# Kernel optimization log

Hardware: AMD Instinct MI355X
Metric: run time of the kernel (lower is better)

The kernel has to match this reference:

```python
import jax, jax.numpy as jnp
import numpy as np

N_NODES = 50000
N_EDGES = 800000
HID = 256
EDGE_DIM = 3


def setup_inputs() -> dict:
    key = jax.random.key(0)
    ks = jax.random.split(key, 10)
    h = jax.random.normal(ks[0], (N_NODES, HID), dtype=jnp.float32)
    edge_index = jax.random.randint(ks[1], (2, N_EDGES), 0, N_NODES, dtype=jnp.int64)
    edge_attr = jax.random.normal(ks[2], (N_EDGES, EDGE_DIM), dtype=jnp.float32)
    # edge_mlp: Linear(3, hid//2) -> SiLU -> Linear(hid//2, 1)
    half = HID // 2
    W1 = jax.random.normal(ks[3], (EDGE_DIM, half), dtype=jnp.float32) / np.sqrt(EDGE_DIM)
    b1 = jnp.zeros((half,), dtype=jnp.float32)
    W2 = jax.random.normal(ks[4], (half, 1), dtype=jnp.float32) / np.sqrt(half)
    b2 = jnp.zeros((1,), dtype=jnp.float32)
    # GCNConv lin (bias=False inside lin; separate additive bias)
    Wc = jax.random.normal(ks[5], (HID, HID), dtype=jnp.float32) / np.sqrt(HID)
    bc = jnp.zeros((HID,), dtype=jnp.float32)
    return {"h": h, "edge_index": edge_index, "edge_attr": edge_attr,
            "W1": W1, "b1": b1, "W2": W2, "b2": b2, "Wc": Wc, "bc": bc}


def reference(h, edge_index, edge_attr, W1, b1, W2, b2, Wc, bc):
    N = h.shape[0]
    # per-edge scalar weight in (0,1): sigmoid(MLP(edge_attr))
    t = jax.nn.silu(edge_attr @ W1 + b1)
    w = jax.nn.sigmoid((t @ W2 + b2)[:, 0])  # [E]

    # add self loops with weight 1.0
    loop = jnp.arange(N, dtype=edge_index.dtype)
    row = jnp.concatenate([edge_index[0], loop])  # sources
    col = jnp.concatenate([edge_index[1], loop])  # targets
    ew = jnp.concatenate([w, jnp.ones((N,), dtype=w.dtype)])

    # symmetric normalization (PyG gcn_norm, flow source_to_target)
    deg = jax.ops.segment_sum(ew, col, num_segments=N)
    dinv = jnp.where(deg > 0, jax.lax.rsqrt(deg), 0.0)
    norm = dinv[row] * ew * dinv[col]  # [E+N]

    # linear transform then gather-scale-scatter aggregation
    x = h @ Wc  # [N, HID]
    msg = x[row] * norm[:, None]  # [E+N, HID]
    out = jax.ops.segment_sum(msg, col, num_segments=N) + bc
    return out
```

## Files before the change

kernel.cpp:

```cpp
#include <hip/hip_runtime.h>

#define NN 50000
#define NE 800000
#define HID 256
#define HALF 128
#define NBLK ((NN + 255) / 256)
#define MT ((NN + 63) / 64)

typedef __attribute__((ext_vector_type(8))) short short8;
typedef __attribute__((ext_vector_type(4))) float floatx4;

__device__ inline unsigned short f2b(float f) {
    unsigned int u = __float_as_uint(f);
    unsigned int r = (u + 0x7FFFu + ((u >> 16) & 1u)) >> 16;
    return (unsigned short)r;
}
__device__ inline float b2f(unsigned int u) {
    return __uint_as_float(u << 16);
}

__global__ __launch_bounds__(256) void k_init(unsigned long long* __restrict__ degq) {
    int n = blockIdx.x * 256 + threadIdx.x;
    if (n < NN) degq[n] = 0ull;
}

__global__ __launch_bounds__(256) void k_convW(const float* __restrict__ Wc,
                                               unsigned short* __restrict__ Wt) {
    int t = blockIdx.x * 256 + threadIdx.x;
    int n = t >> 8, k = t & 255;
    Wt[n * 256 + k] = f2b(Wc[k * 256 + n]);
}

__global__ __launch_bounds__(256) void k_edge_mlp(
    const float* __restrict__ ea, const int* __restrict__ eidx,
    const float* __restrict__ W1, const float* __restrict__ b1,
    const float* __restrict__ W2, const float* __restrict__ b2,
    float* __restrict__ w, unsigned long long* __restrict__ degq) {
    __shared__ float4 wp[HALF];
    __shared__ float w2s[HALF];
    int tid = threadIdx.x;
    if (tid < HALF) {
        wp[tid] = make_float4(W1[tid], W1[HALF + tid], W1[2 * HALF + tid], b1[tid]);
        w2s[tid] = W2[tid];
    }
    __syncthreads();
    int e = blockIdx.x * 256 + tid;
    if (e >= NE) return;
    float a0 = ea[3 * e], a1 = ea[3 * e + 1], a2 = ea[3 * e + 2];
    float acc = b2[0];
#pragma unroll 4
    for (int j = 0; j < HALF; ++j) {
        float4 wv = wp[j];
        float t = fmaf(a0, wv.x, fmaf(a1, wv.y, fmaf(a2, wv.z, wv.w)));
        float s = t * __builtin_amdgcn_rcpf(1.0f + __expf(-t));
        acc = fmaf(s, w2s[j], acc);
    }
    float wv = __builtin_amdgcn_rcpf(1.0f + __expf(-acc));
    w[e] = wv;
    int col = eidx[NE + e];
    unsigned long long q = (1ull << 48) |
        (unsigned long long)__float2uint_rn(wv * 16777216.0f);
    atomicAdd(&degq[col], q);
}

__global__ __launch_bounds__(256) void k_scan_blk(
    const unsigned long long* __restrict__ degq, float* __restrict__ dinv,
    int* __restrict__ off, int* __restrict__ bsum) {
    __shared__ int smem[256];
    int tid = threadIdx.x;
    int idx = blockIdx.x * 256 + tid;
    int v = 0;
    if (idx < NN) {
        unsigned long long q = degq[idx];
        v = (int)(q >> 48);
        float d = fmaf((float)(q & 0xFFFFFFFFFFFFull), 5.9604644775390625e-8f, 1.0f);
        dinv[idx] = rsqrtf(d);
    }
    smem[tid] = v;
    __syncthreads();
#pragma unroll
    for (int s = 1; s < 256; s <<= 1) {
        int t = (tid >= s) ? smem[tid - s] : 0;
        __syncthreads();
        smem[tid] += t;
        __syncthreads();
    }
    if (idx < NN) off[idx] = smem[tid] - v;
    if (tid == 255) bsum[blockIdx.x] = smem[255];
}

__global__ __launch_bounds__(256) void k_scan_top(const int* __restrict__ bsum,
                                                  int* __restrict__ bpre,
                                                  int* __restrict__ off) {
    __shared__ int smem[256];
    int tid = threadIdx.x;
    int v = (tid < NBLK) ? bsum[tid] : 0;
    smem[tid] = v;
    __syncthreads();
#pragma unroll
    for (int s = 1; s < 256; s <<= 1) {
        int t = (tid >= s) ? smem[tid - s] : 0;
        __syncthreads();
        smem[tid] += t;
        __syncthreads();
    }
    if (tid < NBLK) bpre[tid] = smem[tid] - v;
    if (tid == 255) off[NN] = smem[255];
}

__global__ __launch_bounds__(256) void k_scan_add(const int* __restrict__ bpre,
                                                  int* __restrict__ off,
                                                  int* __restrict__ cursor) {
    int idx = blockIdx.x * 256 + threadIdx.x;
    if (idx < NN) {
        int o = off[idx] + bpre[blockIdx.x];
        off[idx] = o;
        cursor[idx] = o;
    }
}

__global__ __launch_bounds__(256) void k_fill(
    const int* __restrict__ eidx, const float* __restrict__ w,
    const float* __restrict__ dinv, int* __restrict__ cursor,
    unsigned int* __restrict__ epk) {
    int e = blockIdx.x * 256 + threadIdx.x;
    if (e >= NE) return;
    int row = eidx[e];
    int col = eidx[NE + e];
    int p = atomicAdd(&cursor[col], 1);
    float nm = dinv[row] * w[e] * dinv[col];
    epk[p] = (unsigned)row | ((unsigned)f2b(nm) << 16);
}

__global__ __launch_bounds__(256) void k_gemm_mfma(
    const float* __restrict__ A, const unsigned short* __restrict__ Wt,
    unsigned short* __restrict__ xh) {
    __shared__ __align__(16) unsigned short As[64][40];
    int tid = threadIdx.x;
    int wave = tid >> 6, lane = tid & 63;
    int mbase = blockIdx.x * 64;
    int nbase = wave * 64;
    int lrow = lane & 15;
    int lg = lane >> 4;
    floatx4 acc[4][4];
#pragma unroll
    for (int t = 0; t < 4; ++t)
#pragma unroll
        for (int u = 0; u < 4; ++u)
            acc[t][u] = (floatx4){0.f, 0.f, 0.f, 0.f};

    int srow = tid >> 2;
    int skg = tid & 3;
    int arow = mbase + srow;
    if (arow >= NN) arow = NN - 1;

    for (int k0 = 0; k0 < 256; k0 += 32) {
        float4 f0 = *(const float4*)&A[arow * 256 + k0 + skg * 8];
        float4 f1 = *(const float4*)&A[arow * 256 + k0 + skg * 8 + 4];
        __syncthreads();
        uint4 pk;
        pk.x = (unsigned)f2b(f0.x) | ((unsigned)f2b(f0.y) << 16);
        pk.y = (unsigned)f2b(f0.z) | ((unsigned)f2b(f0.w) << 16);
        pk.z = (unsigned)f2b(f1.x) | ((unsigned)f2b(f1.y) << 16);
        pk.w = (unsigned)f2b(f1.z) | ((unsigned)f2b(f1.w) << 16);
        *(uint4*)&As[srow][skg * 8] = pk;
        __syncthreads();

        short8 af[4], bf[4];
#pragma unroll
        for (int t = 0; t < 4; ++t)
            af[t] = *(const short8*)&As[t * 16 + lrow][lg * 8];
#pragma unroll
        for (int u = 0; u < 4; ++u)
            bf[u] = *(const short8*)&Wt[(nbase + u * 16 + lrow) * 256 + k0 + lg * 8];
#pragma unroll
        for (int t = 0; t < 4; ++t)
#pragma unroll
            for (int u = 0; u < 4; ++u)
                acc[t][u] = __builtin_amdgcn_mfma_f32_16x16x32_bf16(
                    af[t], bf[u], acc[t][u], 0, 0, 0);
    }
#pragma unroll
    for (int t = 0; t < 4; ++t) {
        int rowb = mbase + t * 16 + lg * 4;
#pragma unroll
        for (int r = 0; r < 4; ++r) {
            int row = rowb + r;
            if (row < NN) {
#pragma unroll
                for (int u = 0; u < 4; ++u)
                    xh[row * 256 + nbase + u * 16 + lrow] = f2b(acc[t][u][r]);
            }
        }
    }
}

__global__ __launch_bounds__(256) void k_aggregate(
    const unsigned short* __restrict__ xh, const int* __restrict__ off,
    const unsigned int* __restrict__ epk, const float* __restrict__ dinv,
    const float* __restrict__ bc, float* __restrict__ out) {
    int n = blockIdx.x * 4 + (threadIdx.x >> 6);
    int lane = threadIdx.x & 63;
    if (n >= NN) return;
    int c4 = lane * 4;
    float di = dinv[n];
    float s = di * di;
    ushort4 xv = *(const ushort4*)&xh[n * 256 + c4];
    float4 bv = *(const float4*)&bc[c4];
    float ax = fmaf(b2f(xv.x), s, bv.x);
    float ay = fmaf(b2f(xv.y), s, bv.y);
    float az = fmaf(b2f(xv.z), s, bv.z);
    float aw = fmaf(b2f(xv.w), s, bv.w);
    int jb = off[n], je = off[n + 1];
    int j = jb;
    for (; j + 4 <= je; j += 4) {
        unsigned p0 = epk[j], p1 = epk[j + 1], p2 = epk[j + 2], p3 = epk[j + 3];
        ushort4 v0 = *(const ushort4*)&xh[(p0 & 0xFFFFu) * 256 + c4];
        ushort4 v1 = *(const ushort4*)&xh[(p1 & 0xFFFFu) * 256 + c4];
        ushort4 v2 = *(const ushort4*)&xh[(p2 & 0xFFFFu) * 256 + c4];
        ushort4 v3 = *(const ushort4*)&xh[(p3 & 0xFFFFu) * 256 + c4];
        float n0 = b2f(p0 >> 16), n1 = b2f(p1 >> 16);
        float n2 = b2f(p2 >> 16), n3 = b2f(p3 >> 16);
        ax = fmaf(b2f(v0.x), n0, ax); ay = fmaf(b2f(v0.y), n0, ay);
        az = fmaf(b2f(v0.z), n0, az); aw = fmaf(b2f(v0.w), n0, aw);
        ax = fmaf(b2f(v1.x), n1, ax); ay = fmaf(b2f(v1.y), n1, ay);
        az = fmaf(b2f(v1.z), n1, az); aw = fmaf(b2f(v1.w), n1, aw);
        ax = fmaf(b2f(v2.x), n2, ax); ay = fmaf(b2f(v2.y), n2, ay);
        az = fmaf(b2f(v2.z), n2, az); aw = fmaf(b2f(v2.w), n2, aw);
        ax = fmaf(b2f(v3.x), n3, ax); ay = fmaf(b2f(v3.y), n3, ay);
        az = fmaf(b2f(v3.z), n3, az); aw = fmaf(b2f(v3.w), n3, aw);
    }
    for (; j < je; ++j) {
        unsigned p = epk[j];
        float nm = b2f(p >> 16);
        ushort4 v = *(const ushort4*)&xh[(p & 0xFFFFu) * 256 + c4];
        ax = fmaf(b2f(v.x), nm, ax); ay = fmaf(b2f(v.y), nm, ay);
        az = fmaf(b2f(v.z), nm, az); aw = fmaf(b2f(v.w), nm, aw);
    }
    *(float4*)&out[n * 256 + c4] = make_float4(ax, ay, az, aw);
}

extern "C" void kernel_launch(void* const* d_in, const int* in_sizes, int n_in,
                              void* d_out, int out_size, void* d_ws, size_t ws_size,
                              hipStream_t stream) {
    const float* h   = (const float*)d_in[0];
    const int* eidx  = (const int*)d_in[1];
    const float* ea  = (const float*)d_in[2];
    const float* W1  = (const float*)d_in[3];
    const float* b1  = (const float*)d_in[4];
    const float* W2  = (const float*)d_in[5];
    const float* b2  = (const float*)d_in[6];
    const float* Wc  = (const float*)d_in[7];
    const float* bc  = (const float*)d_in[8];
    float* out = (float*)d_out;

    char* p = (char*)d_ws;
    float* w                 = (float*)p;              p += (size_t)NE * 4;
    unsigned long long* degq = (unsigned long long*)p; p += (size_t)NN * 8;
    float* dinv              = (float*)p;              p += (size_t)NN * 4;
    unsigned short* xh       = (unsigned short*)p;     p += (size_t)NN * HID * 2;
    unsigned short* Wt       = (unsigned short*)p;     p += (size_t)HID * HID * 2;
    int* off                 = (int*)p;                p += (size_t)(NN + 2) * 4;
    int* cursor              = (int*)p;                p += (size_t)NN * 4;
    unsigned int* epk        = (unsigned int*)p;       p += (size_t)NE * 4;
    int* bsum                = (int*)p;                p += (size_t)NBLK * 4;
    int* bpre                = (int*)p;

    k_init<<<(NN + 255) / 256, 256, 0, stream>>>(degq);
    k_convW<<<(HID * HID) / 256, 256, 0, stream>>>(Wc, Wt);
    k_edge_mlp<<<(NE + 255) / 256, 256, 0, stream>>>(ea, eidx, W1, b1, W2, b2, w, degq);
    k_scan_blk<<<NBLK, 256, 0, stream>>>(degq, dinv, off, bsum);
    k_scan_top<<<1, 256, 0, stream>>>(bsum, bpre, off);
    k_scan_add<<<NBLK, 256, 0, stream>>>(bpre, off, cursor);
    k_fill<<<(NE + 255) / 256, 256, 0, stream>>>(eidx, w, dinv, cursor, epk);
    k_gemm_mfma<<<MT, 256, 0, stream>>>(h, Wt, xh);
    k_aggregate<<<(NN + 3) / 4, 256, 0, stream>>>(xh, off, epk, dinv, bc, out);
}
```

Measured before the change: 303.7 us.

## Fuse setup kernels, stage edge attrs in LDS, widen aggregate gather unroll

Merges the degree-zeroing and weight-transpose kernels into one launch, which removes a launch. The edge MLP now loads edge attributes into shared memory with coalesced float4 loads instead of strided scalar loads. The aggregation loop is unrolled to 8 neighbors, issuing all index and row loads before the FMAs so more gathers are in flight, and it unpacks bf16 pairs from uint2 words. The bounds checks are dropped because NE divides evenly by 256, and zeroing degq relies on the 65536-thread setup grid covering all NN nodes.

```diff
diff --git a/kernel.cpp b/kernel.cpp
--- a/kernel.cpp
+++ b/kernel.cpp
@@ -15,20 +15,16 @@
     unsigned int r = (u + 0x7FFFu + ((u >> 16) & 1u)) >> 16;
     return (unsigned short)r;
 }
-__device__ inline float b2f(unsigned int u) {
-    return __uint_as_float(u << 16);
-}
-
-__global__ __launch_bounds__(256) void k_init(unsigned long long* __restrict__ degq) {
-    int n = blockIdx.x * 256 + threadIdx.x;
-    if (n < NN) degq[n] = 0ull;
-}
-
-__global__ __launch_bounds__(256) void k_convW(const float* __restrict__ Wc,
-                                               unsigned short* __restrict__ Wt) {
+__device__ inline float blo(unsigned u) { return __uint_as_float(u << 16); }
+__device__ inline float bhi(unsigned u) { return __uint_as_float(u & 0xFFFF0000u); }
+
+__global__ __launch_bounds__(256) void k_setup(const float* __restrict__ Wc,
+                                               unsigned short* __restrict__ Wt,
+                                               unsigned long long* __restrict__ degq) {
     int t = blockIdx.x * 256 + threadIdx.x;
     int n = t >> 8, k = t & 255;
     Wt[n * 256 + k] = f2b(Wc[k * 256 + n]);
+    if (t < NN) degq[t] = 0ull;
 }
 
 __global__ __launch_bounds__(256) void k_edge_mlp(
@@ -38,15 +34,17 @@
     float* __restrict__ w, unsigned long long* __restrict__ degq) {
     __shared__ float4 wp[HALF];
     __shared__ float w2s[HALF];
-    int tid = threadIdx.x;
+    __shared__ float eas[768];
+    int tid = threadIdx.x;
+    int e0 = blockIdx.x * 256;
     if (tid < HALF) {
         wp[tid] = make_float4(W1[tid], W1[HALF + tid], W1[2 * HALF + tid], b1[tid]);
         w2s[tid] = W2[tid];
     }
+    if (tid < 192)
+        *(float4*)&eas[tid * 4] = *(const float4*)&ea[(size_t)e0 * 3 + tid * 4];
     __syncthreads();
-    int e = blockIdx.x * 256 + tid;
-    if (e >= NE) return;
-    float a0 = ea[3 * e], a1 = ea[3 * e + 1], a2 = ea[3 * e + 2];
+    float a0 = eas[tid * 3], a1 = eas[tid * 3 + 1], a2 = eas[tid * 3 + 2];
     float acc = b2[0];
 #pragma unroll 4
     for (int j = 0; j < HALF; ++j) {
@@ -55,6 +53,7 @@
         float s = t * __builtin_amdgcn_rcpf(1.0f + __expf(-t));
         acc = fmaf(s, w2s[j], acc);
     }
+    int e = e0 + tid;
     float wv = __builtin_amdgcn_rcpf(1.0f + __expf(-acc));
     w[e] = wv;
     int col = eidx[NE + e];
@@ -202,42 +201,44 @@
     int n = blockIdx.x * 4 + (threadIdx.x >> 6);
     int lane = threadIdx.x & 63;
     if (n >= NN) return;
-    int c4 = lane * 4;
+    const uint2* xt = (const uint2*)xh;
     float di = dinv[n];
     float s = di * di;
-    ushort4 xv = *(const ushort4*)&xh[n * 256 + c4];
-    float4 bv = *(const float4*)&bc[c4];
-    float ax = fmaf(b2f(xv.x), s, bv.x);
-    float ay = fmaf(b2f(xv.y), s, bv.y);
-    float az = fmaf(b2f(xv.z), s, bv.z);
-    float aw = fmaf(b2f(xv.w), s, bv.w);
+    uint2 xv = xt[n * 64 + lane];
+    float4 bv = *(const float4*)&bc[lane * 4];
+    float ax = fmaf(blo(xv.x), s, bv.x);
+    float ay = fmaf(bhi(xv.x), s, bv.y);
+    float az = fmaf(blo(xv.y), s, bv.z);
+    float aw = fmaf(bhi(xv.y), s, bv.w);
     int jb = off[n], je = off[n + 1];
     int j = jb;
-    for (; j + 4 <= je; j += 4) {
-        unsigned p0 = epk[j], p1 = epk[j + 1], p2 = epk[j + 2], p3 = epk[j + 3];
-        ushort4 v0 = *(const ushort4*)&xh[(p0 & 0xFFFFu) * 256 + c4];
-        ushort4 v1 = *(const ushort4*)&xh[(p1 & 0xFFFFu) * 256 + c4];
-        ushort4 v2 = *(const ushort4*)&xh[(p2 & 0xFFFFu) * 256 + c4];
-        ushort4 v3 = *(const ushort4*)&xh[(p3 & 0xFFFFu) * 256 + c4];
-        float n0 = b2f(p0 >> 16), n1 = b2f(p1 >> 16);
-        float n2 = b2f(p2 >> 16), n3 = b2f(p3 >> 16);
-        ax = fmaf(b2f(v0.x), n0, ax); ay = fmaf(b2f(v0.y), n0, ay);
-        az = fmaf(b2f(v0.z), n0, az); aw = fmaf(b2f(v0.w), n0, aw);
-        ax = fmaf(b2f(v1.x), n1, ax); ay = fmaf(b2f(v1.y), n1, ay);
-        az = fmaf(b2f(v1.z), n1, az); aw = fmaf(b2f(v1.w), n1, aw);
-        ax = fmaf(b2f(v2.x), n2, ax); ay = fmaf(b2f(v2.y), n2, ay);
-        az = fmaf(b2f(v2.z), n2, az); aw = fmaf(b2f(v2.w), n2, aw);
-        ax = fmaf(b2f(v3.x), n3, ax); ay = fmaf(b2f(v3.y), n3, ay);
-        az = fmaf(b2f(v3.z), n3, az); aw = fmaf(b2f(v3.w), n3, aw);
+    for (; j + 8 <= je; j += 8) {
+        unsigned pe[8];
+        uint2 g[8];
+#pragma unroll
+        for (int q = 0; q < 8; ++q) pe[q] = epk[j + q];
+#pragma unroll
+        for (int q = 0; q < 8; ++q)
+            g[q] = xt[(pe[q] & 0xFFFFu) * 64 + lane];
+#pragma unroll
+        for (int q = 0; q < 8; ++q) {
+            float nm = bhi(pe[q]);
+            ax = fmaf(blo(g[q].x), nm, ax);
+            ay = fmaf(bhi(g[q].x), nm, ay);
+            az = fmaf(blo(g[q].y), nm, az);
+            aw = fmaf(bhi(g[q].y), nm, aw);
+        }
     }
     for (; j < je; ++j) {
         unsigned p = epk[j];
-        float nm = b2f(p >> 16);
-        ushort4 v = *(const ushort4*)&xh[(p & 0xFFFFu) * 256 + c4];
-        ax = fmaf(b2f(v.x), nm, ax); ay = fmaf(b2f(v.y), nm, ay);
-        az = fmaf(b2f(v.z), nm, az); aw = fmaf(b2f(v.w), nm, aw);
-    }
-    *(float4*)&out[n * 256 + c4] = make_float4(ax, ay, az, aw);
+        float nm = bhi(p);
+        uint2 v = xt[(p & 0xFFFFu) * 64 + lane];
+        ax = fmaf(blo(v.x), nm, ax);
+        ay = fmaf(bhi(v.x), nm, ay);
+        az = fmaf(blo(v.y), nm, az);
+        aw = fmaf(bhi(v.y), nm, aw);
+    }
+    *(float4*)&out[n * 256 + lane * 4] = make_float4(ax, ay, az, aw);
 }
 
 extern "C" void kernel_launch(void* const* d_in, const int* in_sizes, int n_in,
@@ -266,13 +267,12 @@
     int* bsum                = (int*)p;                p += (size_t)NBLK * 4;
     int* bpre                = (int*)p;
 
-    k_init<<<(NN + 255) / 256, 256, 0, stream>>>(degq);
-    k_convW<<<(HID * HID) / 256, 256, 0, stream>>>(Wc, Wt);
-    k_edge_mlp<<<(NE + 255) / 256, 256, 0, stream>>>(ea, eidx, W1, b1, W2, b2, w, degq);
+    k_setup<<<(HID * HID) / 256, 256, 0, stream>>>(Wc, Wt, degq);
+    k_edge_mlp<<<NE / 256, 256, 0, stream>>>(ea, eidx, W1, b1, W2, b2, w, degq);
     k_scan_blk<<<NBLK, 256, 0, stream>>>(degq, dinv, off, bsum);
     k_scan_top<<<1, 256, 0, stream>>>(bsum, bpre, off);
     k_scan_add<<<NBLK, 256, 0, stream>>>(bpre, off, cursor);
-    k_fill<<<(NE + 255) / 256, 256, 0, stream>>>(eidx, w, dinv, cursor, epk);
+    k_fill<<<NE / 256, 256, 0, stream>>>(eidx, w, dinv, cursor, epk);
     k_gemm_mfma<<<MT, 256, 0, stream>>>(h, Wt, xh);
     k_aggregate<<<(NN + 3) / 4, 256, 0, stream>>>(xh, off, epk, dinv, bc, out);
 }
```

Result: no change. 304.1 us (+0.1%).
